# Optimization experiments

Hardware: AMD Instinct MI355X
Metric: run time of the kernel (lower is better)

## Reference

```python
import jax, jax.numpy as jnp
import numpy as np

SHIFT_MIN, SHIFT_MAX = -14.0, 0.0  # deepshift range for weight_bits=5: (-(2**4-2), 0)


def shift_quant(w):
    """Quantize weights to signed powers of two (bit-shift weights), STE form."""
    sign = jnp.sign(w)
    shift = jnp.clip(jnp.round(jnp.log2(jnp.abs(w) + 1e-12)), SHIFT_MIN, SHIFT_MAX)
    q = sign * jnp.exp2(shift)
    return w + jax.lax.stop_gradient(q - w)


def moe_fc(t, wg, w0, b0, w1, b1):
    """Top-1 routing over 2 experts: expert0 dense Linear, expert1 shift-quantized Linear.
    t: [T, C]; weights torch-layout [out, in]. With top_k=1 the softmaxed top-k gate is 1.0,
    so combine is a hard select of the chosen expert's output."""
    logits = t @ wg                      # [T, 2]
    pick0 = (jnp.argmax(logits, axis=-1) == 0)[:, None]
    y0 = t @ w0.T + b0                   # dense expert
    y1 = t @ shift_quant(w1).T + b1      # shift expert
    return jnp.where(pick0, y0, y1)


def setup_inputs() -> dict:
    key = jax.random.key(0)
    ks = jax.random.split(key, 10)
    B, N, C, Dh = 16, 1024, 512, 2048
    s = 0.02
    return {
        "x": jax.random.normal(ks[0], (B, N, C), jnp.float32),
        "H": 32,
        "W": 32,
        "wg1": jax.random.normal(ks[1], (C, 2), jnp.float32) * s,
        "fc1_w0": jax.random.normal(ks[2], (Dh, C), jnp.float32) * s,
        "fc1_b0": jnp.zeros((Dh,), jnp.float32),
        "fc1_w1": jax.random.normal(ks[3], (Dh, C), jnp.float32) * s,
        "fc1_b1": jnp.zeros((Dh,), jnp.float32),
        "dw_w": jax.random.normal(ks[4], (Dh, 1, 3, 3), jnp.float32) * np.sqrt(2.0 / 9.0),
        "dw_b": jnp.zeros((Dh,), jnp.float32),
        "wg2": jax.random.normal(ks[5], (Dh, 2), jnp.float32) * s,
        "fc2_w0": jax.random.normal(ks[6], (C, Dh), jnp.float32) * s,
        "fc2_b0": jnp.zeros((C,), jnp.float32),
        "fc2_w1": jax.random.normal(ks[7], (C, Dh), jnp.float32) * s,
        "fc2_b1": jnp.zeros((C,), jnp.float32),
    }


def reference(x, H, W, wg1, fc1_w0, fc1_b0, fc1_w1, fc1_b1, dw_w, dw_b,
              wg2, fc2_w0, fc2_b0, fc2_w1, fc2_b1):
    B, N, C = x.shape
    Dh = fc1_w0.shape[0]
    # fc1 MoE
    h = moe_fc(x.reshape(-1, C), wg1, fc1_w0, fc1_b0, fc1_w1, fc1_b1)  # [B*N, Dh]
    # DWConv 3x3 depthwise, NCHW
    h = h.reshape(B, N, Dh).transpose(0, 2, 1).reshape(B, Dh, H, W)
    h = jax.lax.conv_general_dilated(
        h, dw_w, window_strides=(1, 1), padding="SAME",
        dimension_numbers=("NCHW", "OIHW", "NCHW"), feature_group_count=Dh)
    h = h + dw_b[None, :, None, None]
    h = h.reshape(B, Dh, N).transpose(0, 2, 1)  # [B, N, Dh]
    # GELU (exact, as nn.GELU default); dropout p=0 -> identity
    h = jax.nn.gelu(h, approximate=False)
    # fc2 MoE
    y = moe_fc(h.reshape(-1, Dh), wg2, fc2_w0, fc2_b0, fc2_w1, fc2_b1)
    return y.reshape(B, N, -1)
```

## Files before the change

kernel.cpp:

```cpp
#include <hip/hip_runtime.h>
#include <hip/hip_bf16.h>


#define TOKS  16384
#define CIN   512
#define DHID  2048

typedef __attribute__((ext_vector_type(8))) __bf16 bf16x8;
typedef __attribute__((ext_vector_type(4))) float  f32x4;
typedef __attribute__((ext_vector_type(4))) float  float4v;
typedef __attribute__((ext_vector_type(4))) unsigned short ushort4v;

__device__ __forceinline__ unsigned short f2bf(float f) {
  union { float f; unsigned int u; } a; a.f = f;
  unsigned int u = a.u;
  unsigned int r = u + 0x7FFFu + ((u >> 16) & 1u);
  return (unsigned short)(r >> 16);
}
__device__ __forceinline__ float bf2f(unsigned short h) {
  union { unsigned int u; float f; } a; a.u = ((unsigned int)h) << 16;
  return a.f;
}

__device__ __forceinline__ float squant(float w) {
  if (w == 0.0f) return 0.0f;
  float aw = fabsf(w) + 1e-12f;
  union { float f; unsigned u; } a; a.f = aw;
  int e = (int)((a.u >> 23) & 0xFFu) - 127;
  unsigned frac = a.u & 0x7FFFFFu;
  int shift = e + (frac >= 0x3504F4u ? 1 : 0);
  shift = min(max(shift, -14), 0);
  union { unsigned u; float f; } q; q.u = (unsigned)(shift + 127) << 23;
  return (w > 0.0f) ? q.f : -q.f;
}

#define GLDS16(gp, lp) __builtin_amdgcn_global_load_lds(                      \
    (const __attribute__((address_space(1))) void*)(gp),                      \
    (__attribute__((address_space(3))) void*)(lp), 16, 0, 0)

__global__ void k_prep(const float* __restrict__ w0, const float* __restrict__ w1,
                       const float* __restrict__ w20, const float* __restrict__ w21,
                       unsigned short* __restrict__ w0hi, unsigned short* __restrict__ w0lo,
                       unsigned short* __restrict__ w1q, unsigned short* __restrict__ w20b,
                       unsigned short* __restrict__ w21b) {
  int i = blockIdx.x * 256 + threadIdx.x;
  if (i >= DHID * CIN) return;
  float v = w0[i];
  unsigned short h = f2bf(v);
  w0hi[i] = h;
  w0lo[i] = f2bf(v - bf2f(h));
  w1q[i]  = f2bf(squant(w1[i]));
  w20b[i] = f2bf(w20[i]);
  w21b[i] = f2bf(squant(w21[i]));
}

__global__ void k_gate1(const float* __restrict__ x, const float* __restrict__ wg1,
                        unsigned char* __restrict__ pick1) {
  int tok = blockIdx.x * 4 + (threadIdx.x >> 6);
  int l = threadIdx.x & 63;
  const float* xr = x + (size_t)tok * CIN;
  float s0 = 0.f, s1 = 0.f;
  for (int i = l; i < CIN; i += 64) {
    float v = xr[i];
    s0 += v * wg1[i * 2 + 0];
    s1 += v * wg1[i * 2 + 1];
  }
  for (int m = 32; m; m >>= 1) { s0 += __shfl_xor(s0, m); s1 += __shfl_xor(s1, m); }
  if (l == 0) pick1[tok] = (s0 >= s1) ? 0 : 1;
}

__global__ void k_scan(const unsigned char* __restrict__ pick, int* __restrict__ perm,
                       int* __restrict__ n0buf) {
  __shared__ int cnt[1024];
  const int t = threadIdx.x;
  unsigned char loc[16];
  int c0 = 0;
  #pragma unroll
  for (int i = 0; i < 16; ++i) { loc[i] = pick[t * 16 + i]; c0 += (loc[i] == 0); }
  cnt[t] = c0;
  __syncthreads();
  for (int off = 1; off < 1024; off <<= 1) {
    int v = cnt[t] + ((t >= off) ? cnt[t - off] : 0);
    __syncthreads();
    cnt[t] = v;
    __syncthreads();
  }
  int total0 = cnt[1023];
  int pre0 = cnt[t] - c0;
  int pre1 = t * 16 - pre0;
  if (t == 0) n0buf[0] = total0;
  int p0 = pre0, p1 = total0 + pre1;
  #pragma unroll
  for (int i = 0; i < 16; ++i) {
    int tok = t * 16 + i;
    if (loc[i] == 0) perm[p0++] = tok; else perm[p1++] = tok;
  }
}

__launch_bounds__(256, 2)
__global__ void k_fc1(const float* __restrict__ x,
                      const unsigned short* __restrict__ w0hi,
                      const unsigned short* __restrict__ w0lo,
                      const unsigned short* __restrict__ w1q,
                      const float* __restrict__ b0, const float* __restrict__ b1,
                      const int* __restrict__ perm, const int* __restrict__ n0buf,
                      float* __restrict__ h32) {
  __shared__ unsigned short lAh[128][40];
  __shared__ unsigned short lAl[128][40];
  __shared__ unsigned short lB0h[128][32];
  __shared__ unsigned short lB0l[128][32];
  __shared__ unsigned short lB1q[128][32];

  const int t = threadIdx.x;
  const int wv = t >> 6, ln = t & 63;
  const int lr = ln & 15, lg = ln >> 4;
  const int tok0 = blockIdx.x * 128;
  const int nbase = blockIdx.y * 128;
  const int wm = (wv >> 1) * 64, wn = (wv & 1) * 64;
  const int n0 = n0buf[0];
  const bool do0 = (tok0 < n0);
  const bool do1 = (tok0 + 128 > n0);

  int prow[4];
  #pragma unroll
  for (int p = 0; p < 4; ++p) prow[p] = perm[tok0 + ((p * 256 + t) >> 3)];

  const int swsrc = ((ln & 3) ^ ((ln >> 3) & 3)) << 3;
  const int swrd  = (lg ^ ((lr >> 1) & 3)) << 3;

  f32x4 acc0[4][4], acc1[4][4];
  #pragma unroll
  for (int i = 0; i < 4; ++i)
    #pragma unroll
    for (int j = 0; j < 4; ++j) {
      acc0[i][j] = f32x4{0.f, 0.f, 0.f, 0.f};
      acc1[i][j] = f32x4{0.f, 0.f, 0.f, 0.f};
    }

  for (int kt = 0; kt < CIN / 32; ++kt) {
    const int k0 = kt * 32;
    float4v av[4];
    #pragma unroll
    for (int p = 0; p < 4; ++p) {
      int idx = p * 256 + t;
      av[p] = *(const float4v*)(x + (size_t)prow[p] * CIN + k0 + ((idx & 7) << 2));
    }
    __syncthreads();
    #pragma unroll
    for (int s = 0; s < 2; ++s) {
      int rowblk = s * 4 + wv;
      int row = (rowblk << 4) + (ln >> 2);
      size_t go = (size_t)(nbase + row) * CIN + k0 + swsrc;
      if (do0) {
        GLDS16(w0hi + go, &lB0h[rowblk << 4][0]);
        GLDS16(w0lo + go, &lB0l[rowblk << 4][0]);
      }
      if (do1) GLDS16(w1q + go, &lB1q[rowblk << 4][0]);
    }
    #pragma unroll
    for (int p = 0; p < 4; ++p) {
      int idx = p * 256 + t;
      int row = idx >> 3, c4 = (idx & 7) << 2;
      ushort4v hv, lv;
      #pragma unroll
      for (int q = 0; q < 4; ++q) {
        float v = av[p][q];
        unsigned short h = f2bf(v);
        hv[q] = h;
        lv[q] = f2bf(v - bf2f(h));
      }
      *(ushort4v*)(&lAh[row][c4]) = hv;
      *(ushort4v*)(&lAl[row][c4]) = lv;
    }
    __syncthreads();

    bf16x8 ah[4], al[4];
    #pragma unroll
    for (int mt = 0; mt < 4; ++mt) {
      ah[mt] = *(const bf16x8*)(&lAh[wm + (mt << 4) + lr][lg << 3]);
      al[mt] = *(const bf16x8*)(&lAl[wm + (mt << 4) + lr][lg << 3]);
    }
    #pragma unroll
    for (int nt = 0; nt < 4; ++nt) {
      int rB = wn + (nt << 4) + lr;
      if (do0) {
        bf16x8 bh = *(const bf16x8*)(&lB0h[rB][swrd]);
        bf16x8 bl = *(const bf16x8*)(&lB0l[rB][swrd]);
        #pragma unroll
        for (int mt = 0; mt < 4; ++mt) {
          acc0[mt][nt] = __builtin_amdgcn_mfma_f32_16x16x32_bf16(ah[mt], bh, acc0[mt][nt], 0, 0, 0);
          acc0[mt][nt] = __builtin_amdgcn_mfma_f32_16x16x32_bf16(al[mt], bh, acc0[mt][nt], 0, 0, 0);
          acc0[mt][nt] = __builtin_amdgcn_mfma_f32_16x16x32_bf16(ah[mt], bl, acc0[mt][nt], 0, 0, 0);
        }
      }
      if (do1) {
        bf16x8 bq = *(const bf16x8*)(&lB1q[rB][swrd]);
        #pragma unroll
        for (int mt = 0; mt < 4; ++mt) {
          acc1[mt][nt] = __builtin_amdgcn_mfma_f32_16x16x32_bf16(ah[mt], bq, acc1[mt][nt], 0, 0, 0);
          acc1[mt][nt] = __builtin_amdgcn_mfma_f32_16x16x32_bf16(al[mt], bq, acc1[mt][nt], 0, 0, 0);
        }
      }
    }
  }
  #pragma unroll
  for (int nt = 0; nt < 4; ++nt) {
    int d = nbase + wn + (nt << 4) + lr;
    float bi0 = b0[d], bi1 = b1[d];
    #pragma unroll
    for (int mt = 0; mt < 4; ++mt) {
      f32x4 v0 = acc0[mt][nt], v1 = acc1[mt][nt];
      #pragma unroll
      for (int rr = 0; rr < 4; ++rr) {
        int pos = tok0 + wm + (mt << 4) + (lg << 2) + rr;
        int tok = perm[pos];
        float val = (pos >= n0) ? (v1[rr] + bi1) : (v0[rr] + bi0);
        h32[(size_t)tok * DHID + d] = val;
      }
    }
  }
}

__global__ void k_conv(const float* __restrict__ h32, const float* __restrict__ dww,
                       const float* __restrict__ dwb, const float* __restrict__ wg2,
                       unsigned short* __restrict__ hb, float* __restrict__ part) {
  __shared__ float tile[10][32][32];
  const int dc = blockIdx.x;
  const int ys = blockIdx.y;
  const int b  = blockIdx.z;
  const int t = threadIdx.x;
  const int d0 = dc * 32, y0 = ys * 8;

  for (int p = 0; p < 10240; p += 256) {
    int idx = p + t;
    int dl = idx & 31, xx = (idx >> 5) & 31, ry = idx >> 10;
    int y = y0 - 1 + ry;
    float v = 0.f;
    if (y >= 0 && y < 32)
      v = h32[(size_t)(b * 1024 + y * 32 + xx) * DHID + d0 + dl];
    tile[ry][xx][dl] = v;
  }
  __syncthreads();

  const int dl = t & 31, xg = t >> 5;
  const int d = d0 + dl;
  float kk[9];
  #pragma unroll
  for (int i = 0; i < 9; ++i) kk[i] = dww[d * 9 + i];
  const float bias = dwb[d];
  const float g0 = wg2[d * 2 + 0], g1 = wg2[d * 2 + 1];

  for (int yy = 0; yy < 8; ++yy) {
    int ry = yy + 1;
    #pragma unroll
    for (int xi = 0; xi < 4; ++xi) {
      int xx = xg * 4 + xi;
      float s = bias;
      #pragma unroll
      for (int dy = -1; dy <= 1; ++dy)
        #pragma unroll
        for (int dx = -1; dx <= 1; ++dx) {
          int xs = xx + dx;
          float v = (xs >= 0 && xs < 32) ? tile[ry + dy][xs][dl] : 0.f;
          s += v * kk[(dy + 1) * 3 + (dx + 1)];
        }
      float gg = 0.5f * s * (1.0f + erff(s * 0.70710678118654752f));
      int tok = b * 1024 + (y0 + yy) * 32 + xx;
      hb[(size_t)tok * DHID + d] = f2bf(gg);
      float p0 = gg * g0, p1 = gg * g1;
      for (int m = 16; m; m >>= 1) { p0 += __shfl_xor(p0, m); p1 += __shfl_xor(p1, m); }
      if (dl == 0) {
        part[(size_t)tok * 128 + dc] = p0;
        part[(size_t)tok * 128 + 64 + dc] = p1;
      }
    }
  }
}

__global__ void k_gate2(const float* __restrict__ part, unsigned char* __restrict__ pick2) {
  int tok = blockIdx.x * 4 + (threadIdx.x >> 6);
  int l = threadIdx.x & 63;
  const float* pr = part + (size_t)tok * 128;
  float s0 = pr[l], s1 = pr[64 + l];
  for (int m = 32; m; m >>= 1) { s0 += __shfl_xor(s0, m); s1 += __shfl_xor(s1, m); }
  if (l == 0) pick2[tok] = (s0 >= s1) ? 0 : 1;
}

__launch_bounds__(256, 2)
__global__ void k_fc2(const unsigned short* __restrict__ hb,
                      const unsigned short* __restrict__ w20b,
                      const unsigned short* __restrict__ w21b,
                      const float* __restrict__ b0, const float* __restrict__ b1,
                      const int* __restrict__ perm, const int* __restrict__ n0buf,
                      float* __restrict__ out) {
  __shared__ unsigned short lA[128][32];
  __shared__ unsigned short lB0[128][32];
  __shared__ unsigned short lB1[128][32];
  const int t = threadIdx.x;
  const int wv = t >> 6, ln = t & 63;
  const int lr = ln & 15, lg = ln >> 4;
  const int tok0 = blockIdx.x * 128;
  const int nbase = blockIdx.y * 128;
  const int wm = (wv >> 1) * 64, wn = (wv & 1) * 64;
  const int n0 = n0buf[0];
  const bool do0 = (tok0 < n0);
  const bool do1 = (tok0 + 128 > n0);

  const int swsrc = ((ln & 3) ^ ((ln >> 3) & 3)) << 3;
  const int swrd  = (lg ^ ((lr >> 1) & 3)) << 3;

  int arow[2];
  #pragma unroll
  for (int s = 0; s < 2; ++s)
    arow[s] = perm[tok0 + ((s * 4 + wv) << 4) + (ln >> 2)];

  f32x4 acc0[4][4], acc1[4][4];
  #pragma unroll
  for (int i = 0; i < 4; ++i)
    #pragma unroll
    for (int j = 0; j < 4; ++j) {
      acc0[i][j] = f32x4{0.f, 0.f, 0.f, 0.f};
      acc1[i][j] = f32x4{0.f, 0.f, 0.f, 0.f};
    }

  for (int kt = 0; kt < DHID / 32; ++kt) {
    const int k0 = kt * 32;
    __syncthreads();
    #pragma unroll
    for (int s = 0; s < 2; ++s) {
      int rowblk = s * 4 + wv;
      int row = (rowblk << 4) + (ln >> 2);
      size_t goB = (size_t)(nbase + row) * DHID + k0 + swsrc;
      GLDS16(hb + (size_t)arow[s] * DHID + k0 + swsrc, &lA[rowblk << 4][0]);
      if (do0) GLDS16(w20b + goB, &lB0[rowblk << 4][0]);
      if (do1) GLDS16(w21b + goB, &lB1[rowblk << 4][0]);
    }
    __syncthreads();
    bf16x8 a[4];
    #pragma unroll
    for (int mt = 0; mt < 4; ++mt)
      a[mt] = *(const bf16x8*)(&lA[wm + (mt << 4) + lr][swrd]);
    #pragma unroll
    for (int nt = 0; nt < 4; ++nt) {
      int rB = wn + (nt << 4) + lr;
      if (do0) {
        bf16x8 b0f = *(const bf16x8*)(&lB0[rB][swrd]);
        #pragma unroll
        for (int mt = 0; mt < 4; ++mt)
          acc0[mt][nt] = __builtin_amdgcn_mfma_f32_16x16x32_bf16(a[mt], b0f, acc0[mt][nt], 0, 0, 0);
      }
      if (do1) {
        bf16x8 b1f = *(const bf16x8*)(&lB1[rB][swrd]);
        #pragma unroll
        for (int mt = 0; mt < 4; ++mt)
          acc1[mt][nt] = __builtin_amdgcn_mfma_f32_16x16x32_bf16(a[mt], b1f, acc1[mt][nt], 0, 0, 0);
      }
    }
  }
  #pragma unroll
  for (int nt = 0; nt < 4; ++nt) {
    int c = nbase + wn + (nt << 4) + lr;
    float bi0 = b0[c], bi1 = b1[c];
    #pragma unroll
    for (int mt = 0; mt < 4; ++mt) {
      f32x4 v0 = acc0[mt][nt], v1 = acc1[mt][nt];
      #pragma unroll
      for (int rr = 0; rr < 4; ++rr) {
        int pos = tok0 + wm + (mt << 4) + (lg << 2) + rr;
        int tok = perm[pos];
        float val = (pos >= n0) ? (v1[rr] + bi1) : (v0[rr] + bi0);
        out[(size_t)tok * CIN + c] = val;
      }
    }
  }
}

extern "C" void kernel_launch(void* const* d_in, const int* in_sizes, int n_in,
                              void* d_out, int out_size, void* d_ws, size_t ws_size,
                              hipStream_t stream) {
  (void)in_sizes; (void)n_in; (void)out_size; (void)ws_size;
  const float* x   = (const float*)d_in[0];
  const float* wg1 = (const float*)d_in[3];
  const float* w0  = (const float*)d_in[4];
  const float* b0  = (const float*)d_in[5];
  const float* w1  = (const float*)d_in[6];
  const float* b1  = (const float*)d_in[7];
  const float* dww = (const float*)d_in[8];
  const float* dwb = (const float*)d_in[9];
  const float* wg2 = (const float*)d_in[10];
  const float* w20 = (const float*)d_in[11];
  const float* b20 = (const float*)d_in[12];
  const float* w21 = (const float*)d_in[13];
  const float* b21 = (const float*)d_in[14];
  float* out = (float*)d_out;

  char* ws = (char*)d_ws;
  const size_t MB2 = 1u << 21;
  unsigned short* w0hi = (unsigned short*)(ws + 0 * MB2);
  unsigned short* w0lo = (unsigned short*)(ws + 1 * MB2);
  unsigned short* w1q  = (unsigned short*)(ws + 2 * MB2);
  unsigned short* w20b = (unsigned short*)(ws + 3 * MB2);
  unsigned short* w21b = (unsigned short*)(ws + 4 * MB2);
  char* p = ws + 5 * MB2;
  unsigned char* pick1 = (unsigned char*)p;            p += 65536;
  unsigned char* pick2 = (unsigned char*)p;            p += 65536;
  int* perm1 = (int*)p;                                p += TOKS * 4;
  int* perm2 = (int*)p;                                p += TOKS * 4;
  int* n0a   = (int*)p;                                p += 256;
  int* n0b   = (int*)p;                                p += 256;
  float* part = (float*)p;                             p += (size_t)TOKS * 128 * 4;
  float* h32  = (float*)p;                             p += (size_t)TOKS * DHID * 4;
  unsigned short* hb = (unsigned short*)p;

  k_prep <<<4096, 256, 0, stream>>>(w0, w1, w20, w21, w0hi, w0lo, w1q, w20b, w21b);
  k_gate1<<<4096, 256, 0, stream>>>(x, wg1, pick1);
  k_scan <<<1, 1024, 0, stream>>>(pick1, perm1, n0a);
  k_fc1  <<<dim3(128, 16), 256, 0, stream>>>(x, w0hi, w0lo, w1q, b0, b1, perm1, n0a, h32);
  k_conv <<<dim3(64, 4, 16), 256, 0, stream>>>(h32, dww, dwb, wg2, hb, part);
  k_gate2<<<4096, 256, 0, stream>>>(part, pick2);
  k_scan <<<1, 1024, 0, stream>>>(pick2, perm2, n0b);
  k_fc2  <<<dim3(128, 4), 256, 0, stream>>>(hb, w20b, w21b, b20, b21, perm2, n0b, out);
}
```

Before: 373.5 us.

## Double-buffer fc1/fc2 LDS with async loads and pre-split x into bf16 hi/lo

Adds a separate kernel that converts x once into bf16 hi/lo arrays, so fc1 can stream A through global-to-LDS direct loads rather than converting in registers every k-step. Both fc1 and fc2 now use a double-buffered LDS layout: the next k-tile is prefetched while the current one is computed, with manual vmcnt waits and barriers in place of two __syncthreads per iteration, plus raised wave priority around the MFMA block. Loads are now issued unconditionally for all experts, adding some wasted bandwidth, and fc1 uses more LDS, which may lower occupancy. The extra prepx pass adds memory traffic for x.

```diff
diff --git a/kernel.cpp b/kernel.cpp
--- a/kernel.cpp
+++ b/kernel.cpp
@@ -54,6 +54,21 @@
   w21b[i] = f2bf(squant(w21[i]));
 }
 
+__global__ void k_prepx(const float* __restrict__ x,
+                        unsigned short* __restrict__ xhi, unsigned short* __restrict__ xlo) {
+  int i = blockIdx.x * 256 + threadIdx.x;
+  float4v v = ((const float4v*)x)[i];
+  ushort4v hv, lv;
+  #pragma unroll
+  for (int q = 0; q < 4; ++q) {
+    unsigned short h = f2bf(v[q]);
+    hv[q] = h;
+    lv[q] = f2bf(v[q] - bf2f(h));
+  }
+  ((ushort4v*)xhi)[i] = hv;
+  ((ushort4v*)xlo)[i] = lv;
+}
+
 __global__ void k_gate1(const float* __restrict__ x, const float* __restrict__ wg1,
                         unsigned char* __restrict__ pick1) {
   int tok = blockIdx.x * 4 + (threadIdx.x >> 6);
@@ -98,35 +113,29 @@
 }
 
 __launch_bounds__(256, 2)
-__global__ void k_fc1(const float* __restrict__ x,
+__global__ void k_fc1(const unsigned short* __restrict__ xhi,
+                      const unsigned short* __restrict__ xlo,
                       const unsigned short* __restrict__ w0hi,
                       const unsigned short* __restrict__ w0lo,
                       const unsigned short* __restrict__ w1q,
                       const float* __restrict__ b0, const float* __restrict__ b1,
                       const int* __restrict__ perm, const int* __restrict__ n0buf,
                       float* __restrict__ h32) {
-  __shared__ unsigned short lAh[128][40];
-  __shared__ unsigned short lAl[128][40];
-  __shared__ unsigned short lB0h[128][32];
-  __shared__ unsigned short lB0l[128][32];
-  __shared__ unsigned short lB1q[128][32];
-
-  const int t = threadIdx.x;
-  const int wv = t >> 6, ln = t & 63;
+  __shared__ unsigned short sm[40960];
+  const int t = threadIdx.x, wv = t >> 6, ln = t & 63;
   const int lr = ln & 15, lg = ln >> 4;
-  const int tok0 = blockIdx.x * 128;
-  const int nbase = blockIdx.y * 128;
+  const int tok0 = blockIdx.x * 128, nbase = blockIdx.y * 128;
   const int wm = (wv >> 1) * 64, wn = (wv & 1) * 64;
   const int n0 = n0buf[0];
-  const bool do0 = (tok0 < n0);
-  const bool do1 = (tok0 + 128 > n0);
-
-  int prow[4];
-  #pragma unroll
-  for (int p = 0; p < 4; ++p) prow[p] = perm[tok0 + ((p * 256 + t) >> 3)];
-
-  const int swsrc = ((ln & 3) ^ ((ln >> 3) & 3)) << 3;
-  const int swrd  = (lg ^ ((lr >> 1) & 3)) << 3;
+  const bool do0 = (tok0 < n0), do1 = (tok0 + 128 > n0);
+
+  int par[2];
+  #pragma unroll
+  for (int s = 0; s < 2; ++s)
+    par[s] = perm[tok0 + ((s * 4 + wv) << 4) + (ln >> 2)];
+
+  const int swsrc = (((ln & 3) ^ ((ln >> 3) & 3)) << 3);
+  const int swrd  = ((lg ^ ((lr >> 1) & 3)) << 3);
 
   f32x4 acc0[4][4], acc1[4][4];
   #pragma unroll
@@ -137,55 +146,38 @@
       acc1[i][j] = f32x4{0.f, 0.f, 0.f, 0.f};
     }
 
-  for (int kt = 0; kt < CIN / 32; ++kt) {
+  auto STAGE = [&](int kt, int db) {
     const int k0 = kt * 32;
-    float4v av[4];
-    #pragma unroll
-    for (int p = 0; p < 4; ++p) {
-      int idx = p * 256 + t;
-      av[p] = *(const float4v*)(x + (size_t)prow[p] * CIN + k0 + ((idx & 7) << 2));
-    }
-    __syncthreads();
     #pragma unroll
     for (int s = 0; s < 2; ++s) {
-      int rowblk = s * 4 + wv;
-      int row = (rowblk << 4) + (ln >> 2);
-      size_t go = (size_t)(nbase + row) * CIN + k0 + swsrc;
+      const int rowblk = s * 4 + wv;
+      const int aoff = db * 8192 + (rowblk << 9);
+      const int boff = 16384 + db * 12288 + (rowblk << 9);
+      size_t ga = (size_t)par[s] * CIN + k0 + swsrc;
+      size_t gb = (size_t)(nbase + (rowblk << 4) + (ln >> 2)) * CIN + k0 + swsrc;
+      GLDS16(xhi + ga, &sm[aoff]);
+      GLDS16(xlo + ga, &sm[aoff + 4096]);
+      GLDS16(w0hi + gb, &sm[boff]);
+      GLDS16(w0lo + gb, &sm[boff + 4096]);
+      GLDS16(w1q + gb, &sm[boff + 8192]);
+    }
+  };
+
+  auto COMPUTE = [&](int db) {
+    bf16x8 ah[4], al[4];
+    #pragma unroll
+    for (int mt = 0; mt < 4; ++mt) {
+      int ro = (wm + (mt << 4) + lr) * 32 + swrd;
+      ah[mt] = *(const bf16x8*)&sm[db * 8192 + ro];
+      al[mt] = *(const bf16x8*)&sm[db * 8192 + 4096 + ro];
+    }
+    __builtin_amdgcn_s_setprio(1);
+    #pragma unroll
+    for (int nt = 0; nt < 4; ++nt) {
+      int bb = 16384 + db * 12288 + (wn + (nt << 4) + lr) * 32 + swrd;
       if (do0) {
-        GLDS16(w0hi + go, &lB0h[rowblk << 4][0]);
-        GLDS16(w0lo + go, &lB0l[rowblk << 4][0]);
-      }
-      if (do1) GLDS16(w1q + go, &lB1q[rowblk << 4][0]);
-    }
-    #pragma unroll
-    for (int p = 0; p < 4; ++p) {
-      int idx = p * 256 + t;
-      int row = idx >> 3, c4 = (idx & 7) << 2;
-      ushort4v hv, lv;
-      #pragma unroll
-      for (int q = 0; q < 4; ++q) {
-        float v = av[p][q];
-        unsigned short h = f2bf(v);
-        hv[q] = h;
-        lv[q] = f2bf(v - bf2f(h));
-      }
-      *(ushort4v*)(&lAh[row][c4]) = hv;
-      *(ushort4v*)(&lAl[row][c4]) = lv;
-    }
-    __syncthreads();
-
-    bf16x8 ah[4], al[4];
-    #pragma unroll
-    for (int mt = 0; mt < 4; ++mt) {
-      ah[mt] = *(const bf16x8*)(&lAh[wm + (mt << 4) + lr][lg << 3]);
-      al[mt] = *(const bf16x8*)(&lAl[wm + (mt << 4) + lr][lg << 3]);
-    }
-    #pragma unroll
-    for (int nt = 0; nt < 4; ++nt) {
-      int rB = wn + (nt << 4) + lr;
-      if (do0) {
-        bf16x8 bh = *(const bf16x8*)(&lB0h[rB][swrd]);
-        bf16x8 bl = *(const bf16x8*)(&lB0l[rB][swrd]);
+        bf16x8 bh = *(const bf16x8*)&sm[bb];
+        bf16x8 bl = *(const bf16x8*)&sm[bb + 4096];
         #pragma unroll
         for (int mt = 0; mt < 4; ++mt) {
           acc0[mt][nt] = __builtin_amdgcn_mfma_f32_16x16x32_bf16(ah[mt], bh, acc0[mt][nt], 0, 0, 0);
@@ -194,7 +186,7 @@
         }
       }
       if (do1) {
-        bf16x8 bq = *(const bf16x8*)(&lB1q[rB][swrd]);
+        bf16x8 bq = *(const bf16x8*)&sm[bb + 8192];
         #pragma unroll
         for (int mt = 0; mt < 4; ++mt) {
           acc1[mt][nt] = __builtin_amdgcn_mfma_f32_16x16x32_bf16(ah[mt], bq, acc1[mt][nt], 0, 0, 0);
@@ -202,7 +194,25 @@
         }
       }
     }
-  }
+    __builtin_amdgcn_s_setprio(0);
+  };
+
+  STAGE(0, 0);
+  #pragma unroll 2
+  for (int kt = 0; kt < 15; ++kt) {
+    __builtin_amdgcn_s_barrier();
+    __builtin_amdgcn_sched_barrier(0);
+    STAGE(kt + 1, (kt + 1) & 1);
+    asm volatile("s_waitcnt vmcnt(10)" ::: "memory");
+    __builtin_amdgcn_s_barrier();
+    __builtin_amdgcn_sched_barrier(0);
+    COMPUTE(kt & 1);
+  }
+  asm volatile("s_waitcnt vmcnt(0)" ::: "memory");
+  __builtin_amdgcn_s_barrier();
+  __builtin_amdgcn_sched_barrier(0);
+  COMPUTE(1);
+
   #pragma unroll
   for (int nt = 0; nt < 4; ++nt) {
     int d = nbase + wn + (nt << 4) + lr;
@@ -293,26 +303,21 @@
                       const float* __restrict__ b0, const float* __restrict__ b1,
                       const int* __restrict__ perm, const int* __restrict__ n0buf,
                       float* __restrict__ out) {
-  __shared__ unsigned short lA[128][32];
-  __shared__ unsigned short lB0[128][32];
-  __shared__ unsigned short lB1[128][32];
-  const int t = threadIdx.x;
-  const int wv = t >> 6, ln = t & 63;
+  __shared__ unsigned short sm[24576];
+  const int t = threadIdx.x, wv = t >> 6, ln = t & 63;
   const int lr = ln & 15, lg = ln >> 4;
-  const int tok0 = blockIdx.x * 128;
-  const int nbase = blockIdx.y * 128;
+  const int tok0 = blockIdx.x * 128, nbase = blockIdx.y * 128;
   const int wm = (wv >> 1) * 64, wn = (wv & 1) * 64;
   const int n0 = n0buf[0];
-  const bool do0 = (tok0 < n0);
-  const bool do1 = (tok0 + 128 > n0);
-
-  const int swsrc = ((ln & 3) ^ ((ln >> 3) & 3)) << 3;
-  const int swrd  = (lg ^ ((lr >> 1) & 3)) << 3;
-
-  int arow[2];
+  const bool do0 = (tok0 < n0), do1 = (tok0 + 128 > n0);
+
+  int par[2];
   #pragma unroll
   for (int s = 0; s < 2; ++s)
-    arow[s] = perm[tok0 + ((s * 4 + wv) << 4) + (ln >> 2)];
+    par[s] = perm[tok0 + ((s * 4 + wv) << 4) + (ln >> 2)];
+
+  const int swsrc = (((ln & 3) ^ ((ln >> 3) & 3)) << 3);
+  const int swrd  = ((lg ^ ((lr >> 1) & 3)) << 3);
 
   f32x4 acc0[4][4], acc1[4][4];
   #pragma unroll
@@ -323,40 +328,62 @@
       acc1[i][j] = f32x4{0.f, 0.f, 0.f, 0.f};
     }
 
-  for (int kt = 0; kt < DHID / 32; ++kt) {
+  auto STAGE = [&](int kt, int db) {
     const int k0 = kt * 32;
-    __syncthreads();
     #pragma unroll
     for (int s = 0; s < 2; ++s) {
-      int rowblk = s * 4 + wv;
-      int row = (rowblk << 4) + (ln >> 2);
-      size_t goB = (size_t)(nbase + row) * DHID + k0 + swsrc;
-      GLDS16(hb + (size_t)arow[s] * DHID + k0 + swsrc, &lA[rowblk << 4][0]);
-      if (do0) GLDS16(w20b + goB, &lB0[rowblk << 4][0]);
-      if (do1) GLDS16(w21b + goB, &lB1[rowblk << 4][0]);
-    }
-    __syncthreads();
+      const int rowblk = s * 4 + wv;
+      const int aoff = db * 4096 + (rowblk << 9);
+      const int boff = 8192 + db * 8192 + (rowblk << 9);
+      size_t ga = (size_t)par[s] * DHID + k0 + swsrc;
+      size_t gb = (size_t)(nbase + (rowblk << 4) + (ln >> 2)) * DHID + k0 + swsrc;
+      GLDS16(hb + ga, &sm[aoff]);
+      GLDS16(w20b + gb, &sm[boff]);
+      GLDS16(w21b + gb, &sm[boff + 4096]);
+    }
+  };
+
+  auto COMPUTE = [&](int db) {
     bf16x8 a[4];
     #pragma unroll
     for (int mt = 0; mt < 4; ++mt)
-      a[mt] = *(const bf16x8*)(&lA[wm + (mt << 4) + lr][swrd]);
+      a[mt] = *(const bf16x8*)&sm[db * 4096 + (wm + (mt << 4) + lr) * 32 + swrd];
+    __builtin_amdgcn_s_setprio(1);
     #pragma unroll
     for (int nt = 0; nt < 4; ++nt) {
-      int rB = wn + (nt << 4) + lr;
+      int bb = 8192 + db * 8192 + (wn + (nt << 4) + lr) * 32 + swrd;
       if (do0) {
-        bf16x8 b0f = *(const bf16x8*)(&lB0[rB][swrd]);
+        bf16x8 b0f = *(const bf16x8*)&sm[bb];
         #pragma unroll
         for (int mt = 0; mt < 4; ++mt)
           acc0[mt][nt] = __builtin_amdgcn_mfma_f32_16x16x32_bf16(a[mt], b0f, acc0[mt][nt], 0, 0, 0);
       }
       if (do1) {
-        bf16x8 b1f = *(const bf16x8*)(&lB1[rB][swrd]);
+        bf16x8 b1f = *(const bf16x8*)&sm[bb + 4096];
         #pragma unroll
         for (int mt = 0; mt < 4; ++mt)
           acc1[mt][nt] = __builtin_amdgcn_mfma_f32_16x16x32_bf16(a[mt], b1f, acc1[mt][nt], 0, 0, 0);
       }
     }
-  }
+    __builtin_amdgcn_s_setprio(0);
+  };
+
+  STAGE(0, 0);
+  #pragma unroll 2
+  for (int kt = 0; kt < 63; ++kt) {
+    __builtin_amdgcn_s_barrier();
+    __builtin_amdgcn_sched_barrier(0);
+    STAGE(kt + 1, (kt + 1) & 1);
+    asm volatile("s_waitcnt vmcnt(6)" ::: "memory");
+    __builtin_amdgcn_s_barrier();
+    __builtin_amdgcn_sched_barrier(0);
+    COMPUTE(kt & 1);
+  }
+  asm volatile("s_waitcnt vmcnt(0)" ::: "memory");
+  __builtin_amdgcn_s_barrier();
+  __builtin_amdgcn_sched_barrier(0);
+  COMPUTE(1);
+
   #pragma unroll
   for (int nt = 0; nt < 4; ++nt) {
     int c = nbase + wn + (nt << 4) + lr;
@@ -402,6 +429,8 @@
   unsigned short* w20b = (unsigned short*)(ws + 3 * MB2);
   unsigned short* w21b = (unsigned short*)(ws + 4 * MB2);
   char* p = ws + 5 * MB2;
+  unsigned short* xhi = (unsigned short*)p;            p += (size_t)TOKS * CIN * 2;
+  unsigned short* xlo = (unsigned short*)p;            p += (size_t)TOKS * CIN * 2;
   unsigned char* pick1 = (unsigned char*)p;            p += 65536;
   unsigned char* pick2 = (unsigned char*)p;            p += 65536;
   int* perm1 = (int*)p;                                p += TOKS * 4;
@@ -413,9 +442,10 @@
   unsigned short* hb = (unsigned short*)p;
 
   k_prep <<<4096, 256, 0, stream>>>(w0, w1, w20, w21, w0hi, w0lo, w1q, w20b, w21b);
+  k_prepx<<<8192, 256, 0, stream>>>(x, xhi, xlo);
   k_gate1<<<4096, 256, 0, stream>>>(x, wg1, pick1);
   k_scan <<<1, 1024, 0, stream>>>(pick1, perm1, n0a);
-  k_fc1  <<<dim3(128, 16), 256, 0, stream>>>(x, w0hi, w0lo, w1q, b0, b1, perm1, n0a, h32);
+  k_fc1  <<<dim3(128, 16), 256, 0, stream>>>(xhi, xlo, w0hi, w0lo, w1q, b0, b1, perm1, n0a, h32);
   k_conv <<<dim3(64, 4, 16), 256, 0, stream>>>(h32, dww, dwb, wg2, hb, part);
   k_gate2<<<4096, 256, 0, stream>>>(part, pick2);
   k_scan <<<1, 1024, 0, stream>>>(pick2, perm2, n0b);
```

After: 441.7 us. +18.3%, slower.
